# Optimization experiments

Hardware: AMD Instinct MI355X
Metric: run time of the kernel (lower is better)

Reference implementation:

```python
import jax, jax.numpy as jnp
import numpy as np

BINS = 10


def setup_inputs() -> dict:
    key = jax.random.key(0)
    k1, k2 = jax.random.split(key)
    N = 16777216
    x = jax.random.normal(k1, (N, 1), dtype=jnp.float32)
    target = jax.random.randint(k2, (N,), 0, 2, dtype=jnp.int32)
    return {"x": x, "target": target}


def reference(x, target):
    # GHMC_Loss forward (binary, num_classes=1), first call (_last_bin_count is None).
    N = x.shape[0]
    logits = x[:, 0]                                   # [N]
    t = target.astype(x.dtype)                         # [N]

    # gradient norm g = |sigmoid(x) - t|  (detached in original)
    g = jnp.abs(jax.nn.sigmoid(logits) - t)            # [N]
    bin_idx = jnp.clip(
        jnp.floor(g * (BINS - 0.0001)).astype(jnp.int32), 0, BINS - 1
    )                                                  # [N]

    # single-pass histogram via scatter-add
    bin_count = jnp.zeros((BINS,), x.dtype).at[bin_idx].add(1.0)
    nonempty = (bin_count > 0).sum().astype(x.dtype)
    gd = jnp.maximum(bin_count * nonempty, 1e-6)
    beta = jnp.asarray(N, x.dtype) / gd                # [BINS]
    weights = beta[bin_idx]                            # [N] gather

    # stable BCE with logits: logaddexp(0, x) - x*t
    ce = jnp.logaddexp(jnp.zeros_like(logits), logits) - logits * t
    return jnp.mean(ce * weights)
```

## Files before the change

### kernel.cpp

```cpp
#include <hip/hip_runtime.h>

#define BINS 10
#define TPB 256
#define MAX_BLOCKS 2048

__device__ __forceinline__ void ghmc_accum(float z, int t, float* ssum, float* scnt) {
    float tf = (float)t;
    float az = fabsf(z);
    float e  = __expf(-az);
    float q  = 1.0f + e;
    float r  = __builtin_amdgcn_rcpf(q);
    float s  = (z >= 0.0f) ? r : e * r;
    float g  = fabsf(s - tf);
    int bin  = (int)(g * 9.9999f);
    bin = bin < (BINS - 1) ? bin : (BINS - 1);
    float ce = fmaxf(z, 0.0f) - z * tf + __logf(q);
    #pragma unroll
    for (int b = 0; b < BINS; ++b) {
        float mf = (bin == b) ? 1.0f : 0.0f;
        ssum[b] = fmaf(mf, ce, ssum[b]);
        scnt[b] += mf;
    }
}

__global__ __launch_bounds__(TPB) void ghmc_main(const float* __restrict__ x,
                                                 const int* __restrict__ tgt,
                                                 float* __restrict__ partial,
                                                 int nvec, int ntotal) {
    float ssum[BINS], scnt[BINS];
    #pragma unroll
    for (int b = 0; b < BINS; ++b) { ssum[b] = 0.0f; scnt[b] = 0.0f; }

    const float4* __restrict__ x4 = (const float4*)x;
    const int4*  __restrict__ t4 = (const int4*)tgt;
    const int tid = threadIdx.x;
    const int stride = gridDim.x * TPB;

    #pragma unroll 2
    for (int gi = blockIdx.x * TPB + tid; gi < nvec; gi += stride) {
        float4 xv = x4[gi];
        int4   tv = t4[gi];
        ghmc_accum(xv.x, tv.x, ssum, scnt);
        ghmc_accum(xv.y, tv.y, ssum, scnt);
        ghmc_accum(xv.z, tv.z, ssum, scnt);
        ghmc_accum(xv.w, tv.w, ssum, scnt);
    }
    if (blockIdx.x == 0) {
        for (int i = nvec * 4 + tid; i < ntotal; i += TPB)
            ghmc_accum(x[i], tgt[i], ssum, scnt);
    }

    #pragma unroll
    for (int b = 0; b < BINS; ++b) {
        #pragma unroll
        for (int o = 32; o > 0; o >>= 1) {
            ssum[b] += __shfl_down(ssum[b], o);
            scnt[b] += __shfl_down(scnt[b], o);
        }
    }
    __shared__ float red[TPB / 64][2 * BINS];
    const int wid = tid >> 6, lane = tid & 63;
    if (lane == 0) {
        #pragma unroll
        for (int b = 0; b < BINS; ++b) {
            red[wid][b]        = ssum[b];
            red[wid][BINS + b] = scnt[b];
        }
    }
    __syncthreads();
    if (tid < 2 * BINS) {
        float v = 0.0f;
        #pragma unroll
        for (int w = 0; w < TPB / 64; ++w) v += red[w][tid];
        partial[blockIdx.x * (2 * BINS) + tid] = v;
    }
}

__global__ __launch_bounds__(TPB) void ghmc_final(const float* __restrict__ partial,
                                                  float* __restrict__ out, int nblocks) {
    float acc[2 * BINS];
    #pragma unroll
    for (int k = 0; k < 2 * BINS; ++k) acc[k] = 0.0f;
    for (int row = threadIdx.x; row < nblocks; row += TPB) {
        const float* p = partial + row * (2 * BINS);
        #pragma unroll
        for (int k = 0; k < 2 * BINS; ++k) acc[k] += p[k];
    }
    #pragma unroll
    for (int k = 0; k < 2 * BINS; ++k) {
        #pragma unroll
        for (int o = 32; o > 0; o >>= 1) acc[k] += __shfl_down(acc[k], o);
    }
    __shared__ float red[TPB / 64][2 * BINS];
    const int wid = threadIdx.x >> 6, lane = threadIdx.x & 63;
    if (lane == 0) {
        #pragma unroll
        for (int k = 0; k < 2 * BINS; ++k) red[wid][k] = acc[k];
    }
    __syncthreads();
    if (threadIdx.x == 0) {
        float ne = 0.0f;
        float sum[BINS], cnt[BINS];
        #pragma unroll
        for (int b = 0; b < BINS; ++b) {
            float s = 0.0f, c = 0.0f;
            #pragma unroll
            for (int w = 0; w < TPB / 64; ++w) { s += red[w][b]; c += red[w][BINS + b]; }
            sum[b] = s; cnt[b] = c;
            ne += (c > 0.0f) ? 1.0f : 0.0f;
        }
        float res = 0.0f;
        #pragma unroll
        for (int b = 0; b < BINS; ++b)
            res += sum[b] / fmaxf(cnt[b] * ne, 1e-6f);
        out[0] = res;
    }
}

extern "C" void kernel_launch(void* const* d_in, const int* in_sizes, int n_in,
                              void* d_out, int out_size, void* d_ws, size_t ws_size,
                              hipStream_t stream) {
    const float* x   = (const float*)d_in[0];
    const int*   tgt = (const int*)d_in[1];
    float* out     = (float*)d_out;
    float* partial = (float*)d_ws;

    int N    = in_sizes[0];
    int nvec = N / 4;

    int blocks = MAX_BLOCKS;
    int maxrows = (int)(ws_size / (2 * BINS * sizeof(float)));
    if (blocks > maxrows) blocks = maxrows;
    int need = (nvec + TPB - 1) / TPB;
    if (blocks > need) blocks = need;
    if (blocks < 1) blocks = 1;

    ghmc_main<<<blocks, TPB, 0, stream>>>(x, tgt, partial, nvec, N);
    ghmc_final<<<1, TPB, 0, stream>>>(partial, out, blocks);
}
```

Baseline: 155.8 us.

## Bin by logit thresholds with cumulative histogram instead of sigmoid binning

```diff
diff --git a/kernel.cpp b/kernel.cpp
--- a/kernel.cpp
+++ b/kernel.cpp
@@ -3,23 +3,25 @@
 #define BINS 10
 #define TPB 256
 #define MAX_BLOCKS 2048
+#define NTHR 9
 
-__device__ __forceinline__ void ghmc_accum(float z, int t, float* ssum, float* scnt) {
-    float tf = (float)t;
-    float az = fabsf(z);
-    float e  = __expf(-az);
+__device__ __constant__ const float c_thr[NTHR] = {
+    -2.1972135f, -1.3862819f, -0.8472836f, -0.4054484f, 2.00002e-5f,
+     0.4054901f,  0.8473312f,  1.3863444f,  2.1973246f
+};
+
+__device__ __forceinline__ void ghmc_accum(float z, int t, float* A, float* C) {
+    unsigned ub = __float_as_uint(z) ^ ((unsigned)t << 31);
+    float u  = __uint_as_float(ub);
+    float e  = __expf(-fabsf(u));
     float q  = 1.0f + e;
-    float r  = __builtin_amdgcn_rcpf(q);
-    float s  = (z >= 0.0f) ? r : e * r;
-    float g  = fabsf(s - tf);
-    int bin  = (int)(g * 9.9999f);
-    bin = bin < (BINS - 1) ? bin : (BINS - 1);
-    float ce = fmaxf(z, 0.0f) - z * tf + __logf(q);
+    float ce = fmaxf(u, 0.0f) + __logf(q);
+    A[0] += ce;
     #pragma unroll
-    for (int b = 0; b < BINS; ++b) {
-        float mf = (bin == b) ? 1.0f : 0.0f;
-        ssum[b] = fmaf(mf, ce, ssum[b]);
-        scnt[b] += mf;
+    for (int k = 1; k <= NTHR; ++k) {
+        float m = (u >= c_thr[k - 1]) ? 1.0f : 0.0f;
+        A[k]    = fmaf(m, ce, A[k]);
+        C[k - 1] += m;
     }
 }
 
@@ -27,9 +29,12 @@
                                                  const int* __restrict__ tgt,
                                                  float* __restrict__ partial,
                                                  int nvec, int ntotal) {
-    float ssum[BINS], scnt[BINS];
+    float A[BINS];
+    float C[NTHR];
     #pragma unroll
-    for (int b = 0; b < BINS; ++b) { ssum[b] = 0.0f; scnt[b] = 0.0f; }
+    for (int b = 0; b < BINS; ++b) A[b] = 0.0f;
+    #pragma unroll
+    for (int k = 0; k < NTHR; ++k) C[k] = 0.0f;
 
     const float4* __restrict__ x4 = (const float4*)x;
     const int4*  __restrict__ t4 = (const int4*)tgt;
@@ -40,35 +45,36 @@
     for (int gi = blockIdx.x * TPB + tid; gi < nvec; gi += stride) {
         float4 xv = x4[gi];
         int4   tv = t4[gi];
-        ghmc_accum(xv.x, tv.x, ssum, scnt);
-        ghmc_accum(xv.y, tv.y, ssum, scnt);
-        ghmc_accum(xv.z, tv.z, ssum, scnt);
-        ghmc_accum(xv.w, tv.w, ssum, scnt);
+        ghmc_accum(xv.x, tv.x, A, C);
+        ghmc_accum(xv.y, tv.y, A, C);
+        ghmc_accum(xv.z, tv.z, A, C);
+        ghmc_accum(xv.w, tv.w, A, C);
     }
     if (blockIdx.x == 0) {
         for (int i = nvec * 4 + tid; i < ntotal; i += TPB)
-            ghmc_accum(x[i], tgt[i], ssum, scnt);
+            ghmc_accum(x[i], tgt[i], A, C);
     }
 
     #pragma unroll
     for (int b = 0; b < BINS; ++b) {
         #pragma unroll
-        for (int o = 32; o > 0; o >>= 1) {
-            ssum[b] += __shfl_down(ssum[b], o);
-            scnt[b] += __shfl_down(scnt[b], o);
-        }
+        for (int o = 32; o > 0; o >>= 1) A[b] += __shfl_down(A[b], o);
+    }
+    #pragma unroll
+    for (int k = 0; k < NTHR; ++k) {
+        #pragma unroll
+        for (int o = 32; o > 0; o >>= 1) C[k] += __shfl_down(C[k], o);
     }
     __shared__ float red[TPB / 64][2 * BINS];
     const int wid = tid >> 6, lane = tid & 63;
     if (lane == 0) {
         #pragma unroll
-        for (int b = 0; b < BINS; ++b) {
-            red[wid][b]        = ssum[b];
-            red[wid][BINS + b] = scnt[b];
-        }
+        for (int b = 0; b < BINS; ++b) red[wid][b] = A[b];
+        #pragma unroll
+        for (int k = 0; k < NTHR; ++k) red[wid][BINS + k] = C[k];
     }
     __syncthreads();
-    if (tid < 2 * BINS) {
+    if (tid < BINS + NTHR) {
         float v = 0.0f;
         #pragma unroll
         for (int w = 0; w < TPB / 64; ++w) v += red[w][tid];
@@ -77,7 +83,8 @@
 }
 
 __global__ __launch_bounds__(TPB) void ghmc_final(const float* __restrict__ partial,
-                                                  float* __restrict__ out, int nblocks) {
+                                                  float* __restrict__ out,
+                                                  int nblocks, int ntotal) {
     float acc[2 * BINS];
     #pragma unroll
     for (int k = 0; k < 2 * BINS; ++k) acc[k] = 0.0f;
@@ -99,20 +106,37 @@
     }
     __syncthreads();
     if (threadIdx.x == 0) {
-        float ne = 0.0f;
-        float sum[BINS], cnt[BINS];
+        float A[BINS + 1], C[BINS + 1];
         #pragma unroll
         for (int b = 0; b < BINS; ++b) {
-            float s = 0.0f, c = 0.0f;
+            float v = 0.0f;
             #pragma unroll
-            for (int w = 0; w < TPB / 64; ++w) { s += red[w][b]; c += red[w][BINS + b]; }
-            sum[b] = s; cnt[b] = c;
+            for (int w = 0; w < TPB / 64; ++w) v += red[w][b];
+            A[b] = v;
+        }
+        A[BINS] = 0.0f;
+        C[0] = (float)ntotal;
+        #pragma unroll
+        for (int k = 1; k <= NTHR; ++k) {
+            float v = 0.0f;
+            #pragma unroll
+            for (int w = 0; w < TPB / 64; ++w) v += red[w][BINS + k - 1];
+            C[k] = v;
+        }
+        C[BINS] = 0.0f;
+        float ne = 0.0f;
+        #pragma unroll
+        for (int b = 0; b < BINS; ++b) {
+            float c = C[b] - C[b + 1];
             ne += (c > 0.0f) ? 1.0f : 0.0f;
         }
         float res = 0.0f;
         #pragma unroll
-        for (int b = 0; b < BINS; ++b)
-            res += sum[b] / fmaxf(cnt[b] * ne, 1e-6f);
+        for (int b = 0; b < BINS; ++b) {
+            float s = A[b] - A[b + 1];
+            float c = C[b] - C[b + 1];
+            res += s / fmaxf(c * ne, 1e-6f);
+        }
         out[0] = res;
     }
 }
@@ -136,5 +160,5 @@
     if (blocks < 1) blocks = 1;
 
     ghmc_main<<<blocks, TPB, 0, stream>>>(x, tgt, partial, nvec, N);
-    ghmc_final<<<1, TPB, 0, stream>>>(partial, out, blocks);
+    ghmc_final<<<1, TPB, 0, stream>>>(partial, out, blocks, N);
 }
```

Result: faster. 152.5 us (-2.1%).
